# Kernel tuning notes

Measured on AMD Instinct MI355X. Metric: run time of the kernel, lower is better.

## Reference

```python
import jax, jax.numpy as jnp
import numpy as np
import math

EPS = 1e-5
K = 4        # conv kernel size
N = 16       # d_state


def setup_inputs() -> dict:
    key = jax.random.key(0)
    b, l, d = 1, 2048, 1024
    di = 2 * d                      # inner channels after split
    dt_rank = math.ceil(d / 16)     # 64
    ks = jax.random.split(key, 8)
    s = 0.02
    return {
        "x": jax.random.normal(ks[0], (b, l, d), jnp.float32),
        "norm_scale": jnp.ones((d,), jnp.float32),
        "w_in": jax.random.normal(ks[1], (d, 4 * d), jnp.float32) * s,
        "conv_w": jax.random.normal(ks[2], (K, 1, di), jnp.float32) * 0.2,
        "conv_b": jnp.zeros((di,), jnp.float32),
        "A_log": jax.random.normal(ks[3], (di, N), jnp.float32) * 0.5,
        "D": jax.random.normal(ks[4], (di,), jnp.float32) * 0.1,
        "w_xproj": jax.random.normal(ks[5], (di, dt_rank + 2 * N), jnp.float32) * s,
        "w_dt": jax.random.normal(ks[6], (dt_rank, di), jnp.float32) * s,
        "b_dt": jnp.zeros((di,), jnp.float32),
        "w_out": jax.random.normal(ks[7], (di, d), jnp.float32) * s,
    }


def _causal_depthwise_conv(x, w, b):
    # x: (b,l,c), w: (K,1,c). Original pads (K-1,K-1) then slices [:, :l] == causal left-pad.
    c = x.shape[-1]
    y = jax.lax.conv_general_dilated(
        x, w, window_strides=(1,), padding=[(K - 1, 0)],
        dimension_numbers=("NWC", "WIO", "NWC"), feature_group_count=c)
    return y + b


def reference(x, norm_scale, w_in, conv_w, conv_b, A_log, D, w_xproj, w_dt, b_dt, w_out):
    dt_rank = w_dt.shape[0]
    # RMSNorm (mean=False, bias=False), scale only
    h = x * jax.lax.rsqrt(jnp.mean(x * x, axis=-1, keepdims=True) + EPS) * norm_scale
    h = h @ w_in                         # (b,l,4d)
    xs, res = jnp.split(h, 2, axis=-1)   # each (b,l,2d)
    res = jax.nn.silu(res)
    xs = jax.nn.silu(_causal_depthwise_conv(xs, conv_w, conv_b))
    proj = xs @ w_xproj                  # (b,l,dt_rank+2N)
    delta, B, C = jnp.split(proj, [dt_rank, dt_rank + N], axis=-1)
    delta = jax.nn.softplus(delta @ w_dt + b_dt)          # (b,l,c)
    A = -jnp.exp(A_log)                                   # (c,n)
    deltaA = jnp.exp(delta[..., None] * A)                # (b,l,c,n)
    deltaBx = (delta * xs)[..., None] * B[:, :, None, :]  # (b,l,c,n)

    def combine(e_i, e_j):
        a_i, b_i = e_i
        a_j, b_j = e_j
        return (a_i * a_j, a_j * b_i + b_j)

    _, ys = jax.lax.associative_scan(combine, (deltaA, deltaBx), axis=1)
    y = jnp.einsum("blcn,bln->blc", ys, C)
    out = (y + xs * D) * res
    return x + out @ w_out
```

## Files before the change

kernel.cpp:

```cpp
#include <hip/hip_runtime.h>

typedef short short8 __attribute__((ext_vector_type(8)));
typedef float floatx4 __attribute__((ext_vector_type(4)));
typedef unsigned int u32;

__device__ __forceinline__ float b2f(unsigned short u) {
    union { unsigned int i; float f; } v; v.i = ((unsigned int)u) << 16; return v.f;
}
__device__ __forceinline__ float hi2f(u32 p) {
    union { unsigned int i; float f; } v; v.i = p & 0xFFFF0000u; return v.f;
}
__device__ __forceinline__ float lo2f(u32 p) {
    union { unsigned int i; float f; } v; v.i = p << 16; return v.f;
}
__device__ __forceinline__ unsigned short f2b(float f) {
    union { unsigned int i; float f; } v; v.f = f;
    unsigned int r = v.i + 0x7FFFu + ((v.i >> 16) & 1u);
    return (unsigned short)(r >> 16);
}
__device__ __forceinline__ float ld(const void* p, size_t i, int f) {
    return f ? ((const float*)p)[i] : b2f(((const unsigned short*)p)[i]);
}
__device__ __forceinline__ int dtf(const void* scale) {
    return (((const unsigned short*)scale)[0] == 0x3F80u) ? 0 : 1;
}
__device__ __forceinline__ void gload16(const unsigned short* g, unsigned short* l) {
    __builtin_amdgcn_global_load_lds(
        (const __attribute__((address_space(1))) u32*)(const void*)g,
        (__attribute__((address_space(3))) u32*)(void*)l, 16, 0, 0);
}
template<int CTRL>
__device__ __forceinline__ float dpp_add(float y) {
    union { float f; int i; } u, r;
    u.f = y;
    r.i = __builtin_amdgcn_update_dpp(0, u.i, CTRL, 0xF, 0xF, true);
    return y + r.f;
}
#define LOG2E 1.44269504f

__global__ __launch_bounds__(256) void prep_kernel(
    const void* x, const void* scale, unsigned short* __restrict__ h,
    const void* w_in, unsigned short* __restrict__ wT,
    const void* w_out, unsigned short* __restrict__ woT)
{
    const int f = dtf(scale);
    const int b = blockIdx.x, tid = threadIdx.x;
    if (b < 2048) {
        const int t = b;
        float xv[4];
        float ss = 0.f;
        #pragma unroll
        for (int j = 0; j < 4; j++) {
            xv[j] = ld(x, (size_t)t * 1024 + j * 256 + tid, f);
            ss += xv[j] * xv[j];
        }
        #pragma unroll
        for (int o = 32; o > 0; o >>= 1) ss += __shfl_down(ss, o);
        __shared__ float sr[4];
        if ((tid & 63) == 0) sr[tid >> 6] = ss;
        __syncthreads();
        float r = rsqrtf((sr[0] + sr[1] + sr[2] + sr[3]) * (1.f / 1024.f) + 1e-5f);
        #pragma unroll
        for (int j = 0; j < 4; j++) {
            int i = j * 256 + tid;
            h[(size_t)t * 1024 + i] = f2b(xv[j] * r * ld(scale, i, f));
        }
    } else if (b < 3072) {
        __shared__ unsigned short tile[64][68];
        const int idx = b - 2048;
        const int n0 = (idx & 63) * 64, k0 = (idx >> 6) * 64;
        #pragma unroll
        for (int j = 0; j < 16; j++) {
            int ii = tid + 256 * j, r = ii >> 6, c = ii & 63;
            tile[r][c] = f2b(ld(w_in, (size_t)(k0 + r) * 4096 + n0 + c, f));
        }
        __syncthreads();
        #pragma unroll
        for (int j = 0; j < 16; j++) {
            int ii = tid + 256 * j, r = ii >> 6, c = ii & 63;
            wT[(size_t)(n0 + r) * 1024 + k0 + c] = tile[c][r];
        }
    } else {
        __shared__ unsigned short tile[64][68];
        const int idx = b - 3072;
        const int n0 = (idx & 15) * 64, k0 = (idx >> 4) * 64;
        #pragma unroll
        for (int j = 0; j < 16; j++) {
            int ii = tid + 256 * j, r = ii >> 6, c = ii & 63;
            tile[r][c] = f2b(ld(w_out, (size_t)(k0 + r) * 1024 + n0 + c, f));
        }
        __syncthreads();
        #pragma unroll
        for (int j = 0; j < 16; j++) {
            int ii = tid + 256 * j, r = ii >> 6, c = ii & 63;
            woT[(size_t)(n0 + r) * 2048 + k0 + c] = tile[c][r];
        }
    }
}

template<int KDIM, int NDIM, int TM, int MODE>
__global__ __launch_bounds__(256) void gemm_bt_kernel(
    const unsigned short* __restrict__ A, const unsigned short* __restrict__ BT,
    void* out0, unsigned short* out1, const void* xres, const void* nscale)
{
    constexpr int RT = TM / 32;
    const int f = dtf(nscale);
    __shared__ __align__(16) unsigned short As[TM * 64];
    __shared__ __align__(16) unsigned short Bs[64 * 64];
    const int t = threadIdx.x, w = t >> 6, lane = t & 63;
    const int q = lane >> 4, low = lane & 15;
    const int row0 = blockIdx.y * TM, n0 = blockIdx.x * 64;
    const int wy = w >> 1, wx = w & 1;

    floatx4 acc[RT][2];
    #pragma unroll
    for (int i = 0; i < RT; i++)
        #pragma unroll
        for (int j = 0; j < 2; j++) acc[i][j] = (floatx4){0.f, 0.f, 0.f, 0.f};

    const int srow = lane >> 3, scol = (lane & 7) * 8;
    const unsigned short* a_src = A + (size_t)(row0 + w * (TM / 4) + srow) * KDIM + scol;
    const unsigned short* b_src = BT + (size_t)(n0 + w * 16 + srow) * KDIM + scol;

    for (int k0 = 0; k0 < KDIM; k0 += 64) {
        #pragma unroll
        for (int i = 0; i < TM / 32; i++)
            gload16(a_src + k0 + i * 8 * KDIM, &As[(w * (TM / 4) + i * 8) * 64]);
        #pragma unroll
        for (int i = 0; i < 2; i++)
            gload16(b_src + k0 + i * 8 * KDIM, &Bs[(w * 16 + i * 8) * 64]);
        __syncthreads();
        #pragma unroll
        for (int kh = 0; kh < 2; kh++) {
            short8 af[RT];
            #pragma unroll
            for (int rt = 0; rt < RT; rt++)
                af[rt] = *(const short8*)&As[(wy * (TM / 2) + rt * 16 + low) * 64 + kh * 32 + q * 8];
            #pragma unroll
            for (int nt = 0; nt < 2; nt++) {
                short8 bf = *(const short8*)&Bs[(wx * 32 + nt * 16 + low) * 64 + kh * 32 + q * 8];
                #pragma unroll
                for (int rt = 0; rt < RT; rt++)
                    acc[rt][nt] = __builtin_amdgcn_mfma_f32_16x16x32_bf16(af[rt], bf, acc[rt][nt], 0, 0, 0);
            }
        }
        __syncthreads();
    }

    #pragma unroll
    for (int nt = 0; nt < 2; nt++) {
        const int col = n0 + wx * 32 + nt * 16 + low;
        #pragma unroll
        for (int rt = 0; rt < RT; rt++) {
            #pragma unroll
            for (int r = 0; r < 4; r++) {
                const int row = row0 + wy * (TM / 2) + rt * 16 + q * 4 + r;
                float v = acc[rt][nt][r];
                if (MODE == 0) {
                    if (col < NDIM / 2) {
                        ((unsigned short*)out0)[(size_t)row * (NDIM / 2) + col] = f2b(v);
                    } else {
                        float s = v / (1.f + __expf(-v));
                        out1[(size_t)row * (NDIM / 2) + (col - NDIM / 2)] = f2b(s);
                    }
                } else {
                    size_t idx = (size_t)row * NDIM + col;
                    float o = v + ld(xres, idx, f);
                    if (f) ((float*)out0)[idx] = o;
                    else   ((unsigned short*)out0)[idx] = f2b(o);
                }
            }
        }
    }
}

__global__ __launch_bounds__(256) void conv_kernel(
    const unsigned short* __restrict__ xs_raw, const void* conv_w,
    const void* conv_b, unsigned short* __restrict__ xs_conv, const void* nscale)
{
    const int f = dtf(nscale);
    int id = blockIdx.x * 256 + threadIdx.x;
    int t = id >> 8, c8 = (id & 255) * 8;
    float acc[8];
    if (f) {
        const float* bf = (const float*)conv_b + c8;
        float4 b0 = *(const float4*)bf, b1 = *(const float4*)(bf + 4);
        acc[0] = b0.x; acc[1] = b0.y; acc[2] = b0.z; acc[3] = b0.w;
        acc[4] = b1.x; acc[5] = b1.y; acc[6] = b1.z; acc[7] = b1.w;
    } else {
        uint4 bv = *(const uint4*)((const unsigned short*)conv_b + c8);
        const unsigned short* bp = (const unsigned short*)&bv;
        #pragma unroll
        for (int j = 0; j < 8; j++) acc[j] = b2f(bp[j]);
    }
    #pragma unroll
    for (int k = 0; k < 4; k++) {
        int tt = t - 3 + k;
        if (tt >= 0) {
            uint4 xv = *(const uint4*)(xs_raw + (size_t)tt * 2048 + c8);
            const unsigned short* xp = (const unsigned short*)&xv;
            float wv[8];
            if (f) {
                const float* wf = (const float*)conv_w + (size_t)k * 2048 + c8;
                float4 w0 = *(const float4*)wf, w1 = *(const float4*)(wf + 4);
                wv[0] = w0.x; wv[1] = w0.y; wv[2] = w0.z; wv[3] = w0.w;
                wv[4] = w1.x; wv[5] = w1.y; wv[6] = w1.z; wv[7] = w1.w;
            } else {
                uint4 wu = *(const uint4*)((const unsigned short*)conv_w + (size_t)k * 2048 + c8);
                const unsigned short* wp = (const unsigned short*)&wu;
                #pragma unroll
                for (int j = 0; j < 8; j++) wv[j] = b2f(wp[j]);
            }
            #pragma unroll
            for (int j = 0; j < 8; j++) acc[j] += wv[j] * b2f(xp[j]);
        }
    }
    unsigned short outv[8];
    #pragma unroll
    for (int j = 0; j < 8; j++) {
        float s = acc[j] / (1.f + __expf(-acc[j]));
        outv[j] = f2b(s);
    }
    *(uint4*)(xs_conv + (size_t)t * 2048 + c8) = *(const uint4*)outv;
}

__global__ __launch_bounds__(256) void xproj_gemm_kernel(
    const unsigned short* __restrict__ A, const void* B,
    float* __restrict__ partials, const void* nscale)
{
    const int f = dtf(nscale);
    __shared__ __align__(16) unsigned short As[64 * 32];
    __shared__ __align__(16) unsigned short Bs[64 * 32];
    const int t = threadIdx.x;
    const int row0 = blockIdx.y * 64, n0 = blockIdx.x * 64;
    const int ks = blockIdx.z;
    const int wave = t >> 6, lane = t & 63;
    const int q = lane >> 4, low = lane & 15;
    floatx4 acc[4];
    #pragma unroll
    for (int i = 0; i < 4; i++) acc[i] = (floatx4){0.f, 0.f, 0.f, 0.f};
    const int ar = t >> 2, ac = (t & 3) * 8;
    const int bk = t >> 3, bn = (t & 7) * 8;
    const int col0 = n0 + bn;
    const int kbeg = ks * 256, kend = kbeg + 256;
    for (int k0 = kbeg; k0 < kend; k0 += 32) {
        uint4 av = *(const uint4*)(A + (size_t)(row0 + ar) * 2048 + k0 + ac);
        *(uint4*)&As[ar * 32 + ac] = av;
        unsigned short bu[8];
        if (col0 < 96) {
            if (f) {
                const float* Bf = (const float*)B + (size_t)(k0 + bk) * 96 + col0;
                float4 b0 = *(const float4*)Bf, b1 = *(const float4*)(Bf + 4);
                bu[0] = f2b(b0.x); bu[1] = f2b(b0.y); bu[2] = f2b(b0.z); bu[3] = f2b(b0.w);
                bu[4] = f2b(b1.x); bu[5] = f2b(b1.y); bu[6] = f2b(b1.z); bu[7] = f2b(b1.w);
            } else {
                uint4 bv = *(const uint4*)((const unsigned short*)B + (size_t)(k0 + bk) * 96 + col0);
                *(uint4*)bu = bv;
            }
        } else {
            #pragma unroll
            for (int j = 0; j < 8; j++) bu[j] = 0;
        }
        #pragma unroll
        for (int j = 0; j < 8; j++) Bs[(bn + j) * 32 + bk] = bu[j];
        __syncthreads();
        short8 af = *(const short8*)&As[(wave * 16 + low) * 32 + q * 8];
        #pragma unroll
        for (int i = 0; i < 4; i++) {
            short8 bfr = *(const short8*)&Bs[(i * 16 + low) * 32 + q * 8];
            acc[i] = __builtin_amdgcn_mfma_f32_16x16x32_bf16(af, bfr, acc[i], 0, 0, 0);
        }
        __syncthreads();
    }
    float* out = partials + (size_t)ks * (2048 * 128);
    #pragma unroll
    for (int i = 0; i < 4; i++) {
        int col = n0 + i * 16 + low;
        #pragma unroll
        for (int r = 0; r < 4; r++) {
            int row = row0 + wave * 16 + q * 4 + r;
            out[(size_t)row * 128 + col] = acc[i][r];
        }
    }
}

__global__ __launch_bounds__(256) void xproj_reduce_kernel(
    const float* __restrict__ partials, float* __restrict__ proj)
{
    int id = blockIdx.x * 256 + threadIdx.x;
    float s = 0.f;
    #pragma unroll
    for (int k = 0; k < 8; k++) s += partials[(size_t)k * (2048 * 128) + id];
    proj[id] = s;
}

__global__ __launch_bounds__(256) void delta_gemm_kernel(
    const float* __restrict__ proj, const void* B, const void* b_dt,
    unsigned short* __restrict__ delta, const void* nscale)
{
    const int f = dtf(nscale);
    __shared__ __align__(16) unsigned short As[64 * 32];
    __shared__ __align__(16) unsigned short Bs[64 * 32];
    const int t = threadIdx.x;
    const int row0 = blockIdx.y * 64, n0 = blockIdx.x * 64;
    const int wave = t >> 6, lane = t & 63;
    const int q = lane >> 4, low = lane & 15;
    floatx4 acc[4];
    #pragma unroll
    for (int i = 0; i < 4; i++) acc[i] = (floatx4){0.f, 0.f, 0.f, 0.f};
    const int ar = t >> 2, ac = (t & 3) * 8;
    const int bk = t >> 3, bn = (t & 7) * 8;
    #pragma unroll
    for (int k0 = 0; k0 < 64; k0 += 32) {
        const float* Ap = proj + (size_t)(row0 + ar) * 128 + k0 + ac;
        float4 a0 = *(const float4*)Ap, a1 = *(const float4*)(Ap + 4);
        As[ar * 32 + ac + 0] = f2b(a0.x); As[ar * 32 + ac + 1] = f2b(a0.y);
        As[ar * 32 + ac + 2] = f2b(a0.z); As[ar * 32 + ac + 3] = f2b(a0.w);
        As[ar * 32 + ac + 4] = f2b(a1.x); As[ar * 32 + ac + 5] = f2b(a1.y);
        As[ar * 32 + ac + 6] = f2b(a1.z); As[ar * 32 + ac + 7] = f2b(a1.w);
        unsigned short bu[8];
        if (f) {
            const float* Bp = (const float*)B + (size_t)(k0 + bk) * 2048 + n0 + bn;
            float4 b0 = *(const float4*)Bp, b1 = *(const float4*)(Bp + 4);
            bu[0] = f2b(b0.x); bu[1] = f2b(b0.y); bu[2] = f2b(b0.z); bu[3] = f2b(b0.w);
            bu[4] = f2b(b1.x); bu[5] = f2b(b1.y); bu[6] = f2b(b1.z); bu[7] = f2b(b1.w);
        } else {
            uint4 bv = *(const uint4*)((const unsigned short*)B + (size_t)(k0 + bk) * 2048 + n0 + bn);
            const unsigned short* bp = (const unsigned short*)&bv;
            #pragma unroll
            for (int j = 0; j < 8; j++) bu[j] = bp[j];
        }
        #pragma unroll
        for (int j = 0; j < 8; j++) Bs[(bn + j) * 32 + bk] = bu[j];
        __syncthreads();
        short8 af = *(const short8*)&As[(wave * 16 + low) * 32 + q * 8];
        #pragma unroll
        for (int i = 0; i < 4; i++) {
            short8 bfr = *(const short8*)&Bs[(i * 16 + low) * 32 + q * 8];
            acc[i] = __builtin_amdgcn_mfma_f32_16x16x32_bf16(af, bfr, acc[i], 0, 0, 0);
        }
        __syncthreads();
    }
    #pragma unroll
    for (int i = 0; i < 4; i++) {
        int col = n0 + i * 16 + low;
        float bias = ld(b_dt, col, f);
        #pragma unroll
        for (int r = 0; r < 4; r++) {
            int row = row0 + wave * 16 + q * 4 + r;
            float v = acc[i][r] + bias;
            float sp = fmaxf(v, 0.f) + log1pf(__expf(-fabsf(v)));
            delta[(size_t)row * 2048 + col] = f2b(sp);
        }
    }
}

__global__ __launch_bounds__(256) void scanA_kernel(
    const unsigned short* __restrict__ delta, const unsigned short* __restrict__ xs,
    const float* __restrict__ proj, const void* A_log,
    float* __restrict__ Aprod, float* __restrict__ Send, const void* nscale)
{
    const int f = dtf(nscale);
    const int chunk = blockIdx.x, c0 = blockIdx.y * 16, t0 = chunk * 64;
    __shared__ __align__(16) u32 dxl[16 * 68];
    __shared__ __align__(16) float Bt[16 * 68];
    const int tid = threadIdx.x;
    #pragma unroll
    for (int j = 0; j < 2; j++) {
        int idx = tid + 256 * j;
        int t = idx >> 3, cp = (idx & 7) * 2;
        u32 dpair = *(const u32*)(delta + (size_t)(t0 + t) * 2048 + c0 + cp);
        u32 xpair = *(const u32*)(xs    + (size_t)(t0 + t) * 2048 + c0 + cp);
        dxl[cp * 68 + t]       = (dpair << 16) | (xpair & 0xFFFFu);
        dxl[(cp + 1) * 68 + t] = (dpair & 0xFFFF0000u) | (xpair >> 16);
    }
    #pragma unroll
    for (int j = 0; j < 4; j++) {
        int idx = tid + 256 * j;
        int t = idx >> 4, n = idx & 15;
        Bt[n * 68 + t] = proj[(size_t)(t0 + t) * 128 + 64 + n];
    }
    __syncthreads();
    const int cl = tid >> 4, n = tid & 15;
    const float A2 = -__expf(ld(A_log, (size_t)(c0 + cl) * 16 + n, f)) * LOG2E;
    float s = 0.f, dsum = 0.f;
    for (int t4 = 0; t4 < 64; t4 += 4) {
        uint4  dx4 = *(const uint4*)&dxl[cl * 68 + t4];
        float4 b4  = *(const float4*)&Bt[n * 68 + t4];
        const u32* dxp = (const u32*)&dx4;
        const float* bp = (const float*)&b4;
        #pragma unroll
        for (int j = 0; j < 4; j++) {
            u32 p = dxp[j];
            float dv = hi2f(p), xv = lo2f(p);
            float a = exp2f(dv * A2);
            s = a * s + dv * xv * bp[j];
            dsum += dv;
        }
    }
    size_t o = (size_t)chunk * 32768 + (size_t)c0 * 16 + tid;
    Aprod[o] = exp2f(A2 * dsum);
    Send[o]  = s;
}

__global__ __launch_bounds__(256) void scanC_kernel(
    const unsigned short* __restrict__ delta, const unsigned short* __restrict__ xs,
    const float* __restrict__ proj, const void* A_log, const void* Dv,
    const float* __restrict__ Aprod, const float* __restrict__ Send,
    const unsigned short* __restrict__ res, unsigned short* __restrict__ inner,
    const void* nscale)
{
    const int f = dtf(nscale);
    const int chunk = blockIdx.x, c0 = blockIdx.y * 16, t0 = chunk * 64;
    __shared__ __align__(16) u32 dxl[16 * 68];
    __shared__ __align__(16) float Bt[16 * 68];
    __shared__ __align__(16) float Ct[16 * 68];
    __shared__ __align__(16) float yl[16 * 68];
    __shared__ float Dl[16];
    const int tid = threadIdx.x;
    if (tid < 16) Dl[tid] = ld(Dv, c0 + tid, f);
    const int g = c0 * 16 + tid;
    float s = 0.f;
    for (int k = 0; k < chunk; k++)
        s = Aprod[(size_t)k * 32768 + g] * s + Send[(size_t)k * 32768 + g];
    #pragma unroll
    for (int j = 0; j < 2; j++) {
        int idx = tid + 256 * j;
        int t = idx >> 3, cp = (idx & 7) * 2;
        u32 dpair = *(const u32*)(delta + (size_t)(t0 + t) * 2048 + c0 + cp);
        u32 xpair = *(const u32*)(xs    + (size_t)(t0 + t) * 2048 + c0 + cp);
        dxl[cp * 68 + t]       = (dpair << 16) | (xpair & 0xFFFFu);
        dxl[(cp + 1) * 68 + t] = (dpair & 0xFFFF0000u) | (xpair >> 16);
    }
    #pragma unroll
    for (int j = 0; j < 4; j++) {
        int idx = tid + 256 * j;
        int t = idx >> 4, n = idx & 15;
        Bt[n * 68 + t] = proj[(size_t)(t0 + t) * 128 + 64 + n];
        Ct[n * 68 + t] = proj[(size_t)(t0 + t) * 128 + 80 + n];
    }
    __syncthreads();
    const int cl = tid >> 4, n = tid & 15;
    const float A2 = -__expf(ld(A_log, (size_t)(c0 + cl) * 16 + n, f)) * LOG2E;
    for (int t4 = 0; t4 < 64; t4 += 4) {
        uint4  dx4 = *(const uint4*)&dxl[cl * 68 + t4];
        float4 b4  = *(const float4*)&Bt[n * 68 + t4];
        float4 c4  = *(const float4*)&Ct[n * 68 + t4];
        const u32* dxp = (const u32*)&dx4;
        const float* bp = (const float*)&b4;
        const float* cp = (const float*)&c4;
        #pragma unroll
        for (int j = 0; j < 4; j++) {
            u32 p = dxp[j];
            float dv = hi2f(p), xv = lo2f(p);
            float a = exp2f(dv * A2);
            s = a * s + dv * xv * bp[j];
            float y = s * cp[j];
            y = dpp_add<0x111>(y);
            y = dpp_add<0x112>(y);
            y = dpp_add<0x114>(y);
            y = dpp_add<0x118>(y);
            if (n == 15) yl[cl * 68 + t4 + j] = y;
        }
    }
    __syncthreads();
    const int et = tid >> 2, ech = (tid & 3) * 4;
    size_t gbase = (size_t)(t0 + et) * 2048 + c0 + ech;
    uint2 rv2 = *(const uint2*)(res + gbase);
    const unsigned short* rp = (const unsigned short*)&rv2;
    unsigned short outv[4];
    #pragma unroll
    for (int j = 0; j < 4; j++) {
        int c = ech + j;
        float y  = yl[c * 68 + et];
        float xv = lo2f(dxl[c * 68 + et]);
        float o  = (y + xv * Dl[c]) * b2f(rp[j]);
        outv[j] = f2b(o);
    }
    *(uint2*)(inner + gbase) = *(const uint2*)outv;
}

extern "C" void kernel_launch(void* const* d_in, const int* in_sizes, int n_in,
                              void* d_out, int out_size, void* d_ws, size_t ws_size,
                              hipStream_t stream) {
    const void* x       = d_in[0];
    const void* nscale  = d_in[1];
    const void* w_in    = d_in[2];
    const void* conv_w  = d_in[3];
    const void* conv_b  = d_in[4];
    const void* A_log   = d_in[5];
    const void* Dv      = d_in[6];
    const void* w_xproj = d_in[7];
    const void* w_dt    = d_in[8];
    const void* b_dt    = d_in[9];
    const void* w_out   = d_in[10];

    char* ws = (char*)d_ws;
    const size_t MB = 1048576;
    unsigned short* xs_raw  = (unsigned short*)(ws);
    unsigned short* res_s   = (unsigned short*)(ws + 8 * MB);
    unsigned short* xs_conv = (unsigned short*)(ws + 16 * MB);
    unsigned short* delta   = (unsigned short*)(ws + 24 * MB);
    unsigned short* h_norm  = (unsigned short*)(ws + 32 * MB);
    unsigned short* wT      = (unsigned short*)(ws + 36 * MB);
    unsigned short* woT     = (unsigned short*)(ws + 44 * MB);
    float*          partials= (float*)(ws + 48 * MB);
    float*          proj    = (float*)(ws + 56 * MB);
    float*          Aprod   = (float*)(ws + 57 * MB);
    float*          Send    = (float*)(ws + 61 * MB);
    unsigned short* inner   = res_s;

    prep_kernel<<<3584, 256, 0, stream>>>(x, nscale, h_norm, w_in, wT, w_out, woT);
    gemm_bt_kernel<1024, 4096, 128, 0><<<dim3(64, 16), 256, 0, stream>>>(
        h_norm, wT, xs_raw, res_s, nullptr, nscale);
    conv_kernel<<<2048, 256, 0, stream>>>(xs_raw, conv_w, conv_b, xs_conv, nscale);
    xproj_gemm_kernel<<<dim3(2, 32, 8), 256, 0, stream>>>(xs_conv, w_xproj, partials, nscale);
    xproj_reduce_kernel<<<1024, 256, 0, stream>>>(partials, proj);
    delta_gemm_kernel<<<dim3(32, 32), 256, 0, stream>>>(proj, w_dt, b_dt, delta, nscale);
    scanA_kernel<<<dim3(32, 128), 256, 0, stream>>>(delta, xs_conv, proj, A_log, Aprod, Send, nscale);
    scanC_kernel<<<dim3(32, 128), 256, 0, stream>>>(delta, xs_conv, proj, A_log, Dv, Aprod, Send, res_s, inner, nscale);
    gemm_bt_kernel<2048, 1024, 64, 1><<<dim3(16, 32), 256, 0, stream>>>(
        inner, woT, d_out, nullptr, x, nscale);
}
```

Measured before the change: 278.0 us.

## Fuse chunked two-pass selective scan into single sequential double-buffered kernel

Replaces the two-kernel chunked scan with one kernel. The old scheme computed per-chunk decay products and end states, then rescanned each chunk with a carried-in prefix state. In the new kernel each block of 16 channels walks all 32 time chunks sequentially, using double-buffered shared-memory tiles with register prefetch of the next chunk. This removes the extra pass over delta, xs and B, the Aprod/Send round trip through global memory and one launch. In exchange, parallelism drops to 128 blocks, each running a 2048-step dependent recurrence, which may leave many CUs idle and make the scan latency-bound.

```diff
diff --git a/kernel.cpp b/kernel.cpp
--- a/kernel.cpp
+++ b/kernel.cpp
@@ -355,129 +355,104 @@
     }
 }
 
-__global__ __launch_bounds__(256) void scanA_kernel(
+__global__ __launch_bounds__(256) void scan_full_kernel(
     const unsigned short* __restrict__ delta, const unsigned short* __restrict__ xs,
-    const float* __restrict__ proj, const void* A_log,
-    float* __restrict__ Aprod, float* __restrict__ Send, const void* nscale)
+    const float* __restrict__ proj, const void* A_log, const void* Dv,
+    const unsigned short* __restrict__ res, unsigned short* __restrict__ inner,
+    const void* nscale)
 {
     const int f = dtf(nscale);
-    const int chunk = blockIdx.x, c0 = blockIdx.y * 16, t0 = chunk * 64;
-    __shared__ __align__(16) u32 dxl[16 * 68];
-    __shared__ __align__(16) float Bt[16 * 68];
+    const int c0 = blockIdx.x * 16;
     const int tid = threadIdx.x;
-    #pragma unroll
-    for (int j = 0; j < 2; j++) {
-        int idx = tid + 256 * j;
-        int t = idx >> 3, cp = (idx & 7) * 2;
-        u32 dpair = *(const u32*)(delta + (size_t)(t0 + t) * 2048 + c0 + cp);
-        u32 xpair = *(const u32*)(xs    + (size_t)(t0 + t) * 2048 + c0 + cp);
-        dxl[cp * 68 + t]       = (dpair << 16) | (xpair & 0xFFFFu);
-        dxl[(cp + 1) * 68 + t] = (dpair & 0xFFFF0000u) | (xpair >> 16);
-    }
-    #pragma unroll
-    for (int j = 0; j < 4; j++) {
-        int idx = tid + 256 * j;
-        int t = idx >> 4, n = idx & 15;
-        Bt[n * 68 + t] = proj[(size_t)(t0 + t) * 128 + 64 + n];
-    }
-    __syncthreads();
+    __shared__ __align__(16) u32 dxl[2][16 * 68];
+    __shared__ __align__(16) float Bt[2][16 * 68], Ct[2][16 * 68];
+    __shared__ __align__(16) float yl[16 * 68];
+    __shared__ float Dl[16];
+    if (tid < 16) Dl[tid] = ld(Dv, c0 + tid, f);
     const int cl = tid >> 4, n = tid & 15;
     const float A2 = -__expf(ld(A_log, (size_t)(c0 + cl) * 16 + n, f)) * LOG2E;
-    float s = 0.f, dsum = 0.f;
-    for (int t4 = 0; t4 < 64; t4 += 4) {
-        uint4  dx4 = *(const uint4*)&dxl[cl * 68 + t4];
-        float4 b4  = *(const float4*)&Bt[n * 68 + t4];
-        const u32* dxp = (const u32*)&dx4;
-        const float* bp = (const float*)&b4;
+
+    u32 dpr[2], xpr[2];
+    float bvr[4], cvr[4];
+    auto issue = [&](int t0) {
+        #pragma unroll
+        for (int j = 0; j < 2; j++) {
+            int idx = tid + 256 * j, t = idx >> 3, cp = (idx & 7) * 2;
+            dpr[j] = *(const u32*)(delta + (size_t)(t0 + t) * 2048 + c0 + cp);
+            xpr[j] = *(const u32*)(xs    + (size_t)(t0 + t) * 2048 + c0 + cp);
+        }
         #pragma unroll
         for (int j = 0; j < 4; j++) {
-            u32 p = dxp[j];
-            float dv = hi2f(p), xv = lo2f(p);
-            float a = exp2f(dv * A2);
-            s = a * s + dv * xv * bp[j];
-            dsum += dv;
-        }
-    }
-    size_t o = (size_t)chunk * 32768 + (size_t)c0 * 16 + tid;
-    Aprod[o] = exp2f(A2 * dsum);
-    Send[o]  = s;
-}
-
-__global__ __launch_bounds__(256) void scanC_kernel(
-    const unsigned short* __restrict__ delta, const unsigned short* __restrict__ xs,
-    const float* __restrict__ proj, const void* A_log, const void* Dv,
-    const float* __restrict__ Aprod, const float* __restrict__ Send,
-    const unsigned short* __restrict__ res, unsigned short* __restrict__ inner,
-    const void* nscale)
-{
-    const int f = dtf(nscale);
-    const int chunk = blockIdx.x, c0 = blockIdx.y * 16, t0 = chunk * 64;
-    __shared__ __align__(16) u32 dxl[16 * 68];
-    __shared__ __align__(16) float Bt[16 * 68];
-    __shared__ __align__(16) float Ct[16 * 68];
-    __shared__ __align__(16) float yl[16 * 68];
-    __shared__ float Dl[16];
-    const int tid = threadIdx.x;
-    if (tid < 16) Dl[tid] = ld(Dv, c0 + tid, f);
-    const int g = c0 * 16 + tid;
+            int idx = tid + 256 * j, t = idx >> 4, nn = idx & 15;
+            bvr[j] = proj[(size_t)(t0 + t) * 128 + 64 + nn];
+            cvr[j] = proj[(size_t)(t0 + t) * 128 + 80 + nn];
+        }
+    };
+    auto commit = [&](int buf) {
+        #pragma unroll
+        for (int j = 0; j < 2; j++) {
+            int idx = tid + 256 * j, t = idx >> 3, cp = (idx & 7) * 2;
+            dxl[buf][cp * 68 + t]       = (dpr[j] << 16) | (xpr[j] & 0xFFFFu);
+            dxl[buf][(cp + 1) * 68 + t] = (dpr[j] & 0xFFFF0000u) | (xpr[j] >> 16);
+        }
+        #pragma unroll
+        for (int j = 0; j < 4; j++) {
+            int idx = tid + 256 * j, t = idx >> 4, nn = idx & 15;
+            Bt[buf][nn * 68 + t] = bvr[j];
+            Ct[buf][nn * 68 + t] = cvr[j];
+        }
+    };
+
+    issue(0);
+    commit(0);
+    __syncthreads();
     float s = 0.f;
-    for (int k = 0; k < chunk; k++)
-        s = Aprod[(size_t)k * 32768 + g] * s + Send[(size_t)k * 32768 + g];
-    #pragma unroll
-    for (int j = 0; j < 2; j++) {
-        int idx = tid + 256 * j;
-        int t = idx >> 3, cp = (idx & 7) * 2;
-        u32 dpair = *(const u32*)(delta + (size_t)(t0 + t) * 2048 + c0 + cp);
-        u32 xpair = *(const u32*)(xs    + (size_t)(t0 + t) * 2048 + c0 + cp);
-        dxl[cp * 68 + t]       = (dpair << 16) | (xpair & 0xFFFFu);
-        dxl[(cp + 1) * 68 + t] = (dpair & 0xFFFF0000u) | (xpair >> 16);
-    }
-    #pragma unroll
-    for (int j = 0; j < 4; j++) {
-        int idx = tid + 256 * j;
-        int t = idx >> 4, n = idx & 15;
-        Bt[n * 68 + t] = proj[(size_t)(t0 + t) * 128 + 64 + n];
-        Ct[n * 68 + t] = proj[(size_t)(t0 + t) * 128 + 80 + n];
-    }
-    __syncthreads();
-    const int cl = tid >> 4, n = tid & 15;
-    const float A2 = -__expf(ld(A_log, (size_t)(c0 + cl) * 16 + n, f)) * LOG2E;
-    for (int t4 = 0; t4 < 64; t4 += 4) {
-        uint4  dx4 = *(const uint4*)&dxl[cl * 68 + t4];
-        float4 b4  = *(const float4*)&Bt[n * 68 + t4];
-        float4 c4  = *(const float4*)&Ct[n * 68 + t4];
-        const u32* dxp = (const u32*)&dx4;
-        const float* bp = (const float*)&b4;
-        const float* cp = (const float*)&c4;
-        #pragma unroll
-        for (int j = 0; j < 4; j++) {
-            u32 p = dxp[j];
-            float dv = hi2f(p), xv = lo2f(p);
-            float a = exp2f(dv * A2);
-            s = a * s + dv * xv * bp[j];
-            float y = s * cp[j];
-            y = dpp_add<0x111>(y);
-            y = dpp_add<0x112>(y);
-            y = dpp_add<0x114>(y);
-            y = dpp_add<0x118>(y);
-            if (n == 15) yl[cl * 68 + t4 + j] = y;
-        }
-    }
-    __syncthreads();
-    const int et = tid >> 2, ech = (tid & 3) * 4;
-    size_t gbase = (size_t)(t0 + et) * 2048 + c0 + ech;
-    uint2 rv2 = *(const uint2*)(res + gbase);
-    const unsigned short* rp = (const unsigned short*)&rv2;
-    unsigned short outv[4];
-    #pragma unroll
-    for (int j = 0; j < 4; j++) {
-        int c = ech + j;
-        float y  = yl[c * 68 + et];
-        float xv = lo2f(dxl[c * 68 + et]);
-        float o  = (y + xv * Dl[c]) * b2f(rp[j]);
-        outv[j] = f2b(o);
-    }
-    *(uint2*)(inner + gbase) = *(const uint2*)outv;
+    int buf = 0;
+    for (int chunk = 0; chunk < 32; chunk++) {
+        const int t0 = chunk * 64;
+        if (chunk < 31) issue(t0 + 64);
+        for (int t4 = 0; t4 < 64; t4 += 4) {
+            uint4  dx4 = *(const uint4*)&dxl[buf][cl * 68 + t4];
+            float4 b4  = *(const float4*)&Bt[buf][n * 68 + t4];
+            float4 c4  = *(const float4*)&Ct[buf][n * 68 + t4];
+            const u32* dxp = (const u32*)&dx4;
+            const float* bp = (const float*)&b4;
+            const float* cp = (const float*)&c4;
+            #pragma unroll
+            for (int j = 0; j < 4; j++) {
+                u32 p = dxp[j];
+                float dv = hi2f(p), xv = lo2f(p);
+                float a = exp2f(dv * A2);
+                s = a * s + dv * xv * bp[j];
+                float y = s * cp[j];
+                y = dpp_add<0x111>(y);
+                y = dpp_add<0x112>(y);
+                y = dpp_add<0x114>(y);
+                y = dpp_add<0x118>(y);
+                if (n == 15) yl[cl * 68 + t4 + j] = y;
+            }
+        }
+        __syncthreads();
+        {
+            const int et = tid >> 2, ech = (tid & 3) * 4;
+            size_t gbase = (size_t)(t0 + et) * 2048 + c0 + ech;
+            uint2 rv2 = *(const uint2*)(res + gbase);
+            const unsigned short* rp = (const unsigned short*)&rv2;
+            unsigned short outv[4];
+            #pragma unroll
+            for (int j = 0; j < 4; j++) {
+                int c = ech + j;
+                float y  = yl[c * 68 + et];
+                float xv = lo2f(dxl[buf][c * 68 + et]);
+                float o  = (y + xv * Dl[c]) * b2f(rp[j]);
+                outv[j] = f2b(o);
+            }
+            *(uint2*)(inner + gbase) = *(const uint2*)outv;
+        }
+        if (chunk < 31) commit(buf ^ 1);
+        __syncthreads();
+        buf ^= 1;
+    }
 }
 
 extern "C" void kernel_launch(void* const* d_in, const int* in_sizes, int n_in,
@@ -506,8 +481,6 @@
     unsigned short* woT     = (unsigned short*)(ws + 44 * MB);
     float*          partials= (float*)(ws + 48 * MB);
     float*          proj    = (float*)(ws + 56 * MB);
-    float*          Aprod   = (float*)(ws + 57 * MB);
-    float*          Send    = (float*)(ws + 61 * MB);
     unsigned short* inner   = res_s;
 
     prep_kernel<<<3584, 256, 0, stream>>>(x, nscale, h_norm, w_in, wT, w_out, woT);
@@ -517,8 +490,7 @@
     xproj_gemm_kernel<<<dim3(2, 32, 8), 256, 0, stream>>>(xs_conv, w_xproj, partials, nscale);
     xproj_reduce_kernel<<<1024, 256, 0, stream>>>(partials, proj);
     delta_gemm_kernel<<<dim3(32, 32), 256, 0, stream>>>(proj, w_dt, b_dt, delta, nscale);
-    scanA_kernel<<<dim3(32, 128), 256, 0, stream>>>(delta, xs_conv, proj, A_log, Aprod, Send, nscale);
-    scanC_kernel<<<dim3(32, 128), 256, 0, stream>>>(delta, xs_conv, proj, A_log, Dv, Aprod, Send, res_s, inner, nscale);
+    scan_full_kernel<<<128, 256, 0, stream>>>(delta, xs_conv, proj, A_log, Dv, res_s, inner, nscale);
     gemm_bt_kernel<2048, 1024, 64, 1><<<dim3(16, 32), 256, 0, stream>>>(
         inner, woT, d_out, nullptr, x, nscale);
 }
```

Result: slower. 393.8 us (+41.7%).
